# Optimization experiments

Measured on AMD Instinct MI355X. Metric: run time of the kernel, lower is better.

The kernel has to match this reference:

```python
import jax, jax.numpy as jnp
import numpy as np

B, N = 16, 65536
N_BOUND = 50           # n_boundaries, linear spacing in [0, 1]
EMBD_LEN = N_BOUND + 1 # 51 learned bucket vectors
EMBD_DIM = 50
OUT_DIM = 50
HID = 2 * EMBD_DIM + 1 # 101, MLP width


def _xavier(key, shape):
    fan_in, fan_out = shape[1], shape[0]
    std = (2.0 / (fan_in + fan_out)) ** 0.5
    return jax.random.normal(key, shape, jnp.float32) * std


def setup_inputs() -> dict:
    key = jax.random.key(0)
    ks = jax.random.split(key, 6)
    x = jax.random.normal(ks[0], (B, N, 1), jnp.float32)
    boundaries = jnp.linspace(0.0, 1.0, N_BOUND).astype(jnp.float32)
    embd = _xavier(ks[1], (EMBD_LEN, EMBD_DIM))
    embd_oob = _xavier(ks[2], (2, OUT_DIM))
    w1 = _xavier(ks[3], (HID, HID))
    b1 = jnp.zeros((HID,), jnp.float32)
    w2 = _xavier(ks[4], (OUT_DIM, HID))
    b2 = jnp.zeros((OUT_DIM,), jnp.float32)
    return {"x": x, "boundaries": boundaries, "embd": embd,
            "embd_oob": embd_oob, "w1": w1, "b1": b1, "w2": w2, "b2": b2}


def reference(x, boundaries, embd, embd_oob, w1, b1, w2, b2):
    xv = x[..., 0]                                   # (B, N)
    # torch.searchsorted default (right=False) == jnp side='left'
    idx = jnp.searchsorted(boundaries, xv)           # in [0, N_BOUND]
    padded = jnp.concatenate([boundaries[:1], boundaries, boundaries[-1:]])  # (N_BOUND+2,)
    lo = padded[idx]
    hi = padded[idx + 1]
    rng = hi - lo
    # rng==0 only where idx is out-of-range (0 or EMBD_LEN-1); those outputs
    # are overwritten below, so guard the division to stay NaN-free.
    dist = (xv - lo) / jnp.where(rng == 0, 1.0, rng)  # (B, N)
    # in-range bucket indices live in [1, EMBD_LEN-2]; clip so idx+1 gather is safe
    ic = jnp.clip(idx, 1, EMBD_LEN - 2)
    feat = jnp.concatenate([embd[ic], embd[ic + 1], dist[..., None]], axis=-1)  # (B, N, 2*EMBD_DIM+1)
    h = jax.nn.gelu(feat @ w1.T + b1, approximate=False)  # torch nn.GELU = exact erf
    mlp_out = h @ w2.T + b2                           # (B, N, OUT_DIM)
    below = (idx == 0)[..., None]
    above = (idx == EMBD_LEN - 1)[..., None]
    out = jnp.where(below, embd_oob[0], jnp.where(above, embd_oob[1], mlp_out))
    return out
```

## Files before the change

### kernel.cpp

```cpp
#include <hip/hip_runtime.h>
#include <math.h>

#define NB        50
#define ED        50
#define OD        50
#define HID       101
#define K         129
#define NBUCKET   49
#define NSAMP     (NBUCKET * K)
#define ROWSTRIDE 52
#define NP        (16 * 65536)
#define CHUNK     17
#define NCHUNK    8

typedef float    f32x2 __attribute__((ext_vector_type(2)));
typedef _Float16 f16x2 __attribute__((ext_vector_type(2)));

__device__ __align__(16) _Float16 g_table[NSAMP * ROWSTRIDE];

__global__ __launch_bounds__(256) void build_table(
    const float* __restrict__ embd,
    const float* __restrict__ w1,
    const float* __restrict__ b1,
    const float* __restrict__ w2,
    const float* __restrict__ b2)
{
    const int blk = blockIdx.x;
    const int t   = threadIdx.x;
    const int bu  = blk >> 3;
    const int ch  = blk & 7;

    __shared__ union U {
        float w1s[HID * HID];
        struct { float w2s[OD * 104]; float hs[CHUNK * 104]; } p;
    } u;
    __shared__ float zc[224];

    for (int i = t; i < HID * HID; i += 256) u.w1s[i] = w1[i];
    __syncthreads();

    if (t < HID) {
        const float* __restrict__ r  = u.w1s + t * HID;
        const float* __restrict__ ea = embd + (bu + 1) * ED;
        float acc = b1[t];
        #pragma unroll 10
        for (int kk = 0; kk < ED; kk++)
            acc = fmaf(ea[kk], r[kk], fmaf(ea[ED + kk], r[ED + kk], acc));
        zc[t]       = acc;
        zc[112 + t] = r[2 * ED];
    }
    __syncthreads();

    for (int i = t; i < OD * HID; i += 256) {
        const int o = i / HID, j = i - o * HID;
        u.p.w2s[o * 104 + j] = w2[i];
    }

    #pragma unroll
    for (int si = 0; si < CHUNK; si++) {
        const int k = ch * CHUNK + si;
        if (t < HID && k < K) {
            const float dist = (float)k * (1.0f / 128.0f);
            const float z = fmaf(dist, zc[112 + t], zc[t]);
            u.p.hs[si * 104 + t] = 0.5f * z * (1.0f + erff(z * 0.70710678118654752f));
        }
    }
    __syncthreads();

    for (int d = t; d < CHUNK * OD; d += 256) {
        const int si = d / OD, o = d - si * OD;
        const int k = ch * CHUNK + si;
        if (k >= K) continue;
        float acc = b2[o];
        const float4* __restrict__ h4 = (const float4*)(u.p.hs  + si * 104);
        const float4* __restrict__ w4 = (const float4*)(u.p.w2s + o  * 104);
        #pragma unroll
        for (int jj = 0; jj < 25; jj++) {
            const float4 hh = h4[jj], ww = w4[jj];
            acc = fmaf(hh.x, ww.x, acc);
            acc = fmaf(hh.y, ww.y, acc);
            acc = fmaf(hh.z, ww.z, acc);
            acc = fmaf(hh.w, ww.w, acc);
        }
        acc = fmaf(u.p.hs[si * 104 + 100], u.p.w2s[o * 104 + 100], acc);
        g_table[(bu * K + k) * ROWSTRIDE + o] = (_Float16)acc;
    }
}

__global__ __launch_bounds__(256) void embed_main(
    const float* __restrict__ x,
    const float* __restrict__ boundaries,
    const float* __restrict__ embd_oob,
    float* __restrict__ out)
{
    __shared__ float sB[NB];
    __shared__ f32x2 sTail[50];
    __shared__ int4  s_pk[256];
    const int t = threadIdx.x;
    if (t < NB) sB[t] = boundaries[t];
    if (t < 2 * OD) ((float*)sTail)[t] = embd_oob[t];
    __syncthreads();

    const int p = blockIdx.x * 256 + t;
    const float xv = x[p];

    int   r0, r1;
    float frac = 0.0f;
    if (xv <= sB[0]) {
        r0 = -1;  r1 = -1;
    } else if (xv > sB[NB - 1]) {
        r0 = -26; r1 = -26;
    } else {
        int j = (int)(xv * 49.0f);
        if (j > 48) j = 48;
        const int idx = (xv > sB[j]) ? ((xv > sB[j + 1]) ? j + 2 : j + 1) : j;
        const float lo = sB[idx - 1];
        const float hi = sB[idx];
        const float dist = (xv - lo) / (hi - lo);
        const float tt = dist * 128.0f;
        int k0 = (int)tt;
        if (k0 > 127) k0 = 127;
        frac = tt - (float)k0;
        const int row = (idx - 1) * K + k0;
        r0 = row * 26; r1 = r0 + 26;
    }
    s_pk[t] = make_int4(r0, r1, __float_as_int(frac), 0);
    __syncthreads();

    const f16x2* __restrict__ tabh = (const f16x2*)g_table;
    f32x2* __restrict__ o2 = (f32x2*)out + (size_t)blockIdx.x * 6400;

    #pragma unroll
    for (int i = 0; i < 25; i++) {
        const int e  = i * 256 + t;
        const int pt = e / 25;
        const int c2 = e - pt * 25;
        const int4 pk = s_pk[pt];
        f32x2 r;
        if (pk.x >= 0) {
            const float fr = __int_as_float(pk.z);
            const f16x2 a = tabh[pk.x + c2];
            const f16x2 b = tabh[pk.y + c2];
            const float ax = (float)a.x, ay = (float)a.y;
            r.x = fmaf(fr, (float)b.x - ax, ax);
            r.y = fmaf(fr, (float)b.y - ay, ay);
        } else {
            r = sTail[c2 - pk.x - 1];
        }
        o2[e] = r;
    }
}

extern "C" void kernel_launch(void* const* d_in, const int* in_sizes, int n_in,
                              void* d_out, int out_size, void* d_ws, size_t ws_size,
                              hipStream_t stream) {
    const float* x    = (const float*)d_in[0];
    const float* bnd  = (const float*)d_in[1];
    const float* embd = (const float*)d_in[2];
    const float* oob  = (const float*)d_in[3];
    const float* w1   = (const float*)d_in[4];
    const float* b1   = (const float*)d_in[5];
    const float* w2   = (const float*)d_in[6];
    const float* b2   = (const float*)d_in[7];
    float* out = (float*)d_out;

    build_table<<<NBUCKET * NCHUNK, 256, 0, stream>>>(embd, w1, b1, w2, b2);
    embed_main<<<NP / 256, 256, 0, stream>>>(x, bnd, oob, out);
}
```

Baseline: 237.9 us.

## Use persistent grid-stride blocks and 16-byte vector output stores in embed_main

The launch drops from 4096 blocks to 1024 persistent blocks, each looping over four 256-point regions so per-block setup (boundary and OOB loads into shared memory) is amortized. Output writes are widened from 8-byte f32x2 stores to 16-byte f32x4 stores, each assembling two half-pairs that may span two points. This targets store efficiency on the write-bound output stream, at the cost of extra index arithmetic, a branch at point boundaries, and fewer resident blocks to hide latency.

```diff
diff --git a/kernel.cpp b/kernel.cpp
--- a/kernel.cpp
+++ b/kernel.cpp
@@ -12,8 +12,11 @@
 #define NP        (16 * 65536)
 #define CHUNK     17
 #define NCHUNK    8
+#define NBLK      1024
+#define NREG      (NP / 256 / NBLK)
 
 typedef float    f32x2 __attribute__((ext_vector_type(2)));
+typedef float    f32x4 __attribute__((ext_vector_type(4)));
 typedef _Float16 f16x2 __attribute__((ext_vector_type(2)));
 
 __device__ __align__(16) _Float16 g_table[NSAMP * ROWSTRIDE];
@@ -87,6 +90,24 @@
     }
 }
 
+__device__ __forceinline__ f32x2 half_val(const int4 pk, int c2,
+                                          const f16x2* __restrict__ tabh,
+                                          const f32x2* sTail)
+{
+    f32x2 r;
+    if (pk.x >= 0) {
+        const float fr = __int_as_float(pk.z);
+        const f16x2 a = tabh[pk.x + c2];
+        const f16x2 b = tabh[pk.y + c2];
+        const float ax = (float)a.x, ay = (float)a.y;
+        r.x = fmaf(fr, (float)b.x - ax, ax);
+        r.y = fmaf(fr, (float)b.y - ay, ay);
+    } else {
+        r = sTail[c2 - pk.x - 1];
+    }
+    return r;
+}
+
 __global__ __launch_bounds__(256) void embed_main(
     const float* __restrict__ x,
     const float* __restrict__ boundaries,
@@ -99,55 +120,68 @@
     const int t = threadIdx.x;
     if (t < NB) sB[t] = boundaries[t];
     if (t < 2 * OD) ((float*)sTail)[t] = embd_oob[t];
-    __syncthreads();
-
-    const int p = blockIdx.x * 256 + t;
-    const float xv = x[p];
-
-    int   r0, r1;
-    float frac = 0.0f;
-    if (xv <= sB[0]) {
-        r0 = -1;  r1 = -1;
-    } else if (xv > sB[NB - 1]) {
-        r0 = -26; r1 = -26;
-    } else {
-        int j = (int)(xv * 49.0f);
-        if (j > 48) j = 48;
-        const int idx = (xv > sB[j]) ? ((xv > sB[j + 1]) ? j + 2 : j + 1) : j;
-        const float lo = sB[idx - 1];
-        const float hi = sB[idx];
-        const float dist = (xv - lo) / (hi - lo);
-        const float tt = dist * 128.0f;
-        int k0 = (int)tt;
-        if (k0 > 127) k0 = 127;
-        frac = tt - (float)k0;
-        const int row = (idx - 1) * K + k0;
-        r0 = row * 26; r1 = r0 + 26;
-    }
-    s_pk[t] = make_int4(r0, r1, __float_as_int(frac), 0);
-    __syncthreads();
 
     const f16x2* __restrict__ tabh = (const f16x2*)g_table;
-    f32x2* __restrict__ o2 = (f32x2*)out + (size_t)blockIdx.x * 6400;
-
-    #pragma unroll
-    for (int i = 0; i < 25; i++) {
-        const int e  = i * 256 + t;
-        const int pt = e / 25;
-        const int c2 = e - pt * 25;
-        const int4 pk = s_pk[pt];
-        f32x2 r;
-        if (pk.x >= 0) {
-            const float fr = __int_as_float(pk.z);
-            const f16x2 a = tabh[pk.x + c2];
-            const f16x2 b = tabh[pk.y + c2];
-            const float ax = (float)a.x, ay = (float)a.y;
-            r.x = fmaf(fr, (float)b.x - ax, ax);
-            r.y = fmaf(fr, (float)b.y - ay, ay);
+
+    for (int reg = 0; reg < NREG; reg++) {
+        const int pbase = (reg * NBLK + blockIdx.x) * 256;
+        __syncthreads();
+
+        const float xv = x[pbase + t];
+        int   r0, r1;
+        float frac = 0.0f;
+        if (xv <= sB[0]) {
+            r0 = -1;  r1 = -1;
+        } else if (xv > sB[NB - 1]) {
+            r0 = -26; r1 = -26;
         } else {
-            r = sTail[c2 - pk.x - 1];
-        }
-        o2[e] = r;
+            int j = (int)(xv * 49.0f);
+            if (j > 48) j = 48;
+            const int idx = (xv > sB[j]) ? ((xv > sB[j + 1]) ? j + 2 : j + 1) : j;
+            const float lo = sB[idx - 1];
+            const float hi = sB[idx];
+            const float dist = (xv - lo) / (hi - lo);
+            const float tt = dist * 128.0f;
+            int k0 = (int)tt;
+            if (k0 > 127) k0 = 127;
+            frac = tt - (float)k0;
+            const int row = (idx - 1) * K + k0;
+            r0 = row * 26; r1 = r0 + 26;
+        }
+        s_pk[t] = make_int4(r0, r1, __float_as_int(frac), 0);
+        __syncthreads();
+
+        f32x4* __restrict__ o4 = (f32x4*)(out + (size_t)pbase * OD);
+
+        #pragma unroll
+        for (int it = 0; it < 12; it++) {
+            const int e4 = it * 256 + t;
+            const int f  = 4 * e4;
+            const int pt = f / 50;
+            const int c  = f - 50 * pt;
+            const int cA = c >> 1;
+            const int4 pkA = s_pk[pt];
+            const f32x2 rA = half_val(pkA, cA, tabh, sTail);
+            f32x2 rB;
+            if (c < 48) rB = half_val(pkA, cA + 1, tabh, sTail);
+            else        rB = half_val(s_pk[pt + 1], 0, tabh, sTail);
+            f32x4 v; v.x = rA.x; v.y = rA.y; v.z = rB.x; v.w = rB.y;
+            o4[e4] = v;
+        }
+        if (t < 128) {
+            const int e4 = 12 * 256 + t;
+            const int f  = 4 * e4;
+            const int pt = f / 50;
+            const int c  = f - 50 * pt;
+            const int cA = c >> 1;
+            const int4 pkA = s_pk[pt];
+            const f32x2 rA = half_val(pkA, cA, tabh, sTail);
+            f32x2 rB;
+            if (c < 48) rB = half_val(pkA, cA + 1, tabh, sTail);
+            else        rB = half_val(s_pk[pt + 1], 0, tabh, sTail);
+            f32x4 v; v.x = rA.x; v.y = rA.y; v.z = rB.x; v.w = rB.y;
+            o4[e4] = v;
+        }
     }
 }
 
@@ -165,5 +199,5 @@
     float* out = (float*)d_out;
 
     build_table<<<NBUCKET * NCHUNK, 256, 0, stream>>>(embd, w1, b1, w2, b2);
-    embed_main<<<NP / 256, 256, 0, stream>>>(x, bnd, oob, out);
-}
+    embed_main<<<NBLK, 256, 0, stream>>>(x, bnd, oob, out);
+}
```

Result: slower. 260.2 us (+9.4%).
